# Kernel tuning notes

Measured on AMD Instinct MI355X. Metric: run time of the kernel, lower is better.

## Reference

```python
import jax, jax.numpy as jnp
import numpy as np

# --- model dims (from init args) ---
LAYERS = 6
LEAF = 2 ** (LAYERS - 1)        # 32
M_LEN = 128
CAM_NUM = 2
MAIN_CAM = 0
LATENT = 48
H_LAT = 2048                    # LatentNet hidden
H_BR = 512                      # ChooseBranchNet hidden
B = 16384

# Path bits: for leaf i, bit at classifier depth d (root->leaf order) is
# (i >> (LAYERS-2-d)) & 1. This is exactly what the search_table + double
# advanced-indexing gather in the torch code computes (heap tree routing).
_BITS = ((np.arange(LEAF)[:, None] >> np.arange(LAYERS - 2, -1, -1)[None, :]) & 1)  # [LEAF, LAYERS-1]
BITS = jnp.asarray(_BITS, dtype=jnp.int32)


def setup_inputs() -> dict:
    key = jax.random.key(0)
    ks = jax.random.split(key, 9)
    s = lambda fan: 1.0 / np.sqrt(fan)
    return {
        "batch_data": jax.random.normal(ks[0], (B, CAM_NUM, M_LEN), dtype=jnp.float32),
        # LatentNet: [B, 2*M_LEN] -> hidden -> LEAF*LATENT
        "Wl1": jax.random.normal(ks[1], (2 * M_LEN, H_LAT), dtype=jnp.float32) * s(2 * M_LEN),
        "bl1": jnp.zeros((H_LAT,), dtype=jnp.float32),
        "Wl2": jax.random.normal(ks[2], (H_LAT, LEAF * LATENT), dtype=jnp.float32) * s(H_LAT),
        "bl2": jnp.zeros((LEAF * LATENT,), dtype=jnp.float32),
        # ChooseBranchNet (shared across the LAYERS-1 classifier slots): M_LEN -> hidden -> 2
        "Wb1": jax.random.normal(ks[3], (M_LEN, H_BR), dtype=jnp.float32) * s(M_LEN),
        "bb1": jnp.zeros((H_BR,), dtype=jnp.float32),
        "Wb2": jax.random.normal(ks[4], (H_BR, 2), dtype=jnp.float32) * s(H_BR),
        "bb2": jnp.zeros((2,), dtype=jnp.float32),
    }


def reference(batch_data, Wl1, bl1, Wl2, bl2, Wb1, bb1, Wb2, bb2):
    bsz = batch_data.shape[0]
    # expand_measurements: main cam repeated (LAYERS-1) times -> [B, LAYERS-1, M_LEN]
    main = batch_data[:, MAIN_CAM]                                  # [B, M_LEN]
    x_br = jnp.broadcast_to(main[:, None, :], (bsz, LAYERS - 1, M_LEN))
    # ChooseBranchNet -> per-layer 2-way probabilities
    h = jax.nn.relu(jnp.einsum('blm,mh->blh', x_br, Wb1) + bb1)
    p = jax.nn.softmax(jnp.einsum('blh,ho->blo', h, Wb2) + bb2, axis=-1)  # [B, L-1, 2]
    # Tree gates: product of path-branch probabilities along root->leaf path.
    comp = jnp.where(BITS[None] == 1, p[:, None, :, 1], p[:, None, :, 0])  # [B, LEAF, L-1]
    gates = jnp.prod(comp, axis=-1)                                        # [B, LEAF]
    # top-1 routing (argsort(...)[:, -1] as in the torch code)
    router = jnp.argsort(gates, axis=-1)[:, -1]                            # [B]
    # LatentNet on concatenated two-camera measurements
    x2 = jnp.concatenate([batch_data[:, 0], batch_data[:, 1]], axis=-1)    # [B, 2*M_LEN]
    hl = jax.nn.relu(x2 @ Wl1 + bl1)
    nn_latent = (hl @ Wl2 + bl2).reshape(bsz, LEAF, LATENT)
    # scatter-select per-sample leaf latent (replaces the torch.where loop)
    select = jnp.take_along_axis(nn_latent, router[:, None, None], axis=1)[:, 0]  # [B, LATENT]
    return select
```

## Files before the change

kernel.cpp:

```cpp
#include <hip/hip_runtime.h>
#include <stdint.h>

typedef short bf16x8 __attribute__((ext_vector_type(8)));
typedef float f32x4 __attribute__((ext_vector_type(4)));

#define NROWS 16384
#define K1DIM 256
#define N1DIM 2048
#define N2DIM 96
#define MARGIN 0.03f

#define GLD16(g, l) __builtin_amdgcn_global_load_lds( \
    (const __attribute__((address_space(1))) uint32_t*)(g), \
    (__attribute__((address_space(3))) uint32_t*)(l), 16, 0, 0)

__device__ __forceinline__ ushort f2bf(float x) {
  union { float f; uint32_t u; } c; c.f = x;
  uint32_t u = c.u;
  return (ushort)((u + 0x7FFFu + ((u >> 16) & 1u)) >> 16);
}

__global__ __launch_bounds__(256) void k0_convert(
    const float* __restrict__ bd, const float* __restrict__ Wl1,
    const float* __restrict__ Wl2, const float* __restrict__ Wb1,
    ushort* __restrict__ x2bf, ushort* __restrict__ wl1t,
    ushort* __restrict__ w2t, ushort* __restrict__ wb1t) {
  int i = blockIdx.x * 256 + threadIdx.x;
  {
    float4 v = ((const float4*)bd)[i];
    ushort4 o;
    o.x = f2bf(v.x); o.y = f2bf(v.y); o.z = f2bf(v.z); o.w = f2bf(v.w);
    ((ushort4*)x2bf)[i] = o;
  }
  if (i < 2048 * 256) {
    int n = i >> 8, k = i & 255;
    wl1t[i] = f2bf(Wl1[k * 2048 + n]);
  }
  if (i < 96 * 2048) {
    int j = i >> 11, k = i & 2047;
    int col = (j < 48) ? j : (1440 + j);
    w2t[i] = f2bf(Wl2[k * 1536 + col]);
  }
  if (i < 512 * 128) {
    int j = i >> 7, m = i & 127;
    wb1t[i] = f2bf(Wb1[m * 512 + j]);
  }
}

__global__ __launch_bounds__(256) void k1a_score(
    const ushort* __restrict__ x2bf, const ushort* __restrict__ wb1t,
    const float* __restrict__ bb1, const float* __restrict__ Wb2,
    float* __restrict__ part) {
  __shared__ __align__(1024) ushort As[128 * 64];
  __shared__ __align__(1024) ushort Bs[128 * 64];
  const int t = threadIdx.x, ln = t & 63, wv = t >> 6;
  const int m0 = blockIdx.y << 7;
  const int n0 = blockIdx.x << 7;
  const int wm = (wv >> 1) << 6, wn = (wv & 1) << 6;
  const int rsub = ln >> 3, kc8 = ln & 7;
  const int q = ln >> 4, rr = ln & 15;

  f32x4 acc[4][4] = {};

  for (int k0 = 0; k0 < 128; k0 += 64) {
#pragma unroll
    for (int i = 0; i < 4; i++) {
      int inst = (wv << 2) + i;
      int row = (inst << 3) + rsub;
      GLD16(x2bf + (size_t)(m0 + row) * 256 + k0 + (kc8 << 3), As + (inst << 9));
      GLD16(wb1t + (size_t)(n0 + row) * 128 + k0 + (kc8 << 3), Bs + (inst << 9));
    }
    __syncthreads();
#pragma unroll
    for (int kk = 0; kk < 2; kk++) {
      int kb = ((kk << 2) + q) << 3;
      bf16x8 af[4], bfr[4];
#pragma unroll
      for (int mi = 0; mi < 4; mi++)
        af[mi] = *(const bf16x8*)(As + (((wm + (mi << 4) + rr)) << 6) + kb);
#pragma unroll
      for (int ni = 0; ni < 4; ni++)
        bfr[ni] = *(const bf16x8*)(Bs + (((wn + (ni << 4) + rr)) << 6) + kb);
#pragma unroll
      for (int mi = 0; mi < 4; mi++)
#pragma unroll
        for (int ni = 0; ni < 4; ni++)
          acc[mi][ni] = __builtin_amdgcn_mfma_f32_16x16x32_bf16(
              af[mi], bfr[ni], acc[mi][ni], 0, 0, 0);
    }
    __syncthreads();
  }

  float s4[4][4] = {};
#pragma unroll
  for (int ni = 0; ni < 4; ni++) {
    int col = n0 + wn + (ni << 4) + rr;
    float bias = bb1[col];
    float wdv = Wb2[col * 2 + 1] - Wb2[col * 2];
#pragma unroll
    for (int mi = 0; mi < 4; mi++) {
      f32x4 a = acc[mi][ni];
#pragma unroll
      for (int v = 0; v < 4; v++)
        s4[mi][v] += fmaxf(a[v] + bias, 0.f) * wdv;
    }
  }
#pragma unroll
  for (int off = 1; off <= 8; off <<= 1)
#pragma unroll
    for (int mi = 0; mi < 4; mi++)
#pragma unroll
      for (int v = 0; v < 4; v++)
        s4[mi][v] += __shfl_xor(s4[mi][v], off);

  if (rr == 0) {
    float* dst = part + (size_t)(blockIdx.x * 2 + (wv & 1)) * NROWS +
                 m0 + wm + (q << 2);
#pragma unroll
    for (int mi = 0; mi < 4; mi++) {
      float4 v4 = make_float4(s4[mi][0], s4[mi][1], s4[mi][2], s4[mi][3]);
      *(float4*)(dst + (mi << 4)) = v4;
    }
  }
}

__global__ __launch_bounds__(256) void k1b_classify(
    const float* __restrict__ part, const float* __restrict__ bb2,
    int* __restrict__ router, int* __restrict__ list, int* __restrict__ counter) {
  int t = blockIdx.x * 256 + threadIdx.x;
  float s = bb2[1] - bb2[0];
#pragma unroll
  for (int i = 0; i < 8; i++) s += part[i * NROWS + t];
  router[t] = (s >= 0.f) ? 1 : 0;
  if (fabsf(s) < MARGIN) {
    int idx = atomicAdd(counter, 1);
    list[idx] = t;
  }
}

__global__ __launch_bounds__(256) void k1c_recheck(
    const float* __restrict__ bd, const float* __restrict__ Wb1,
    const float* __restrict__ Wb2, const float* __restrict__ bb1,
    const float* __restrict__ bb2, const int* __restrict__ list,
    const int* __restrict__ counter, int* __restrict__ router) {
  const int ln = threadIdx.x & 63;
  const int wid = (blockIdx.x * 256 + threadIdx.x) >> 6;
  const int count = *counter;
  const float c = bb2[1] - bb2[0];

  for (int base = wid * 4; base < count; base += 512 * 4) {
    int rows[4];
#pragma unroll
    for (int r = 0; r < 4; r++) {
      int idx = base + r;
      rows[r] = list[(idx < count) ? idx : base];
    }
    float acc[4][8];
#pragma unroll
    for (int r = 0; r < 4; r++)
#pragma unroll
      for (int u = 0; u < 8; u++) acc[r][u] = 0.f;

    for (int m = 0; m < 128; m++) {
      float w[8];
#pragma unroll
      for (int u = 0; u < 8; u++) w[u] = Wb1[m * 512 + (u << 6) + ln];
#pragma unroll
      for (int r = 0; r < 4; r++) {
        float x = bd[(size_t)rows[r] * 256 + m];
#pragma unroll
        for (int u = 0; u < 8; u++) acc[r][u] = fmaf(x, w[u], acc[r][u]);
      }
    }
    float sc[4];
#pragma unroll
    for (int r = 0; r < 4; r++) {
      float s = 0.f;
#pragma unroll
      for (int u = 0; u < 8; u++) {
        int j = (u << 6) + ln;
        float wd = Wb2[j * 2 + 1] - Wb2[j * 2];
        s += fmaxf(acc[r][u] + bb1[j], 0.f) * wd;
      }
#pragma unroll
      for (int off = 1; off <= 32; off <<= 1) s += __shfl_xor(s, off);
      sc[r] = s + c;
    }
    if (ln == 0) {
#pragma unroll
      for (int r = 0; r < 4; r++)
        if (base + r < count) router[rows[r]] = (sc[r] >= 0.f) ? 1 : 0;
    }
  }
}

__global__ __launch_bounds__(256, 2) void k2_fused(
    const ushort* __restrict__ x2bf, const ushort* __restrict__ wl1t,
    const ushort* __restrict__ w2t, const float* __restrict__ bl1,
    const float* __restrict__ bl2, const int* __restrict__ router,
    float* __restrict__ out) {
  __shared__ __align__(1024) ushort Bsm[16384];
  __shared__ __align__(1024) ushort Asm[8192];
  __shared__ __align__(1024) ushort Wsm[12288];
  ushort* Hs = Bsm;
  const int t = threadIdx.x, ln = t & 63, wv = t >> 6;
  const int ks2 = blockIdx.x;
  const int m0 = blockIdx.y << 6;
  const int q = ln >> 4, rr = ln & 15;
  const int sr4 = ln >> 4;
  const int s16 = ln & 15;

  f32x4 accP[6] = {};

  for (int nc = 0; nc < 8; nc++) {
    const int n0 = (ks2 << 10) + (nc << 7);

#pragma unroll
    for (int j = 0; j < 6; j++) {
      int inst = wv * 6 + j;
      int r = (inst << 2) + sr4;
      int c = s16 ^ (r & 7);
      GLD16(w2t + (size_t)r * 2048 + n0 + (c << 3), Wsm + (inst << 9));
    }

    f32x4 acc1[4][2] = {};
#pragma unroll 1
    for (int ks = 0; ks < 2; ks++) {
      const int kg = ks << 7;
#pragma unroll
      for (int i = 0; i < 4; i++) {
        int inst = (wv << 2) + i;
        int r = (inst << 2) + sr4;
        int c = s16 ^ (r & 7);
        GLD16(x2bf + (size_t)(m0 + r) * K1DIM + kg + (c << 3),
              Asm + (inst << 9));
      }
#pragma unroll
      for (int i = 0; i < 8; i++) {
        int inst = (wv << 3) + i;
        int r = (inst << 2) + sr4;
        int c = s16 ^ (r & 7);
        GLD16(wl1t + (size_t)(n0 + r) * K1DIM + kg + (c << 3),
              Bsm + (inst << 9));
      }
      __syncthreads();
#pragma unroll
      for (int kk = 0; kk < 4; kk++) {
        int c = (kk << 2) + q;
        int sl = (c ^ (rr & 7)) << 3;
        bf16x8 af[4], bfr[2];
#pragma unroll
        for (int mi = 0; mi < 4; mi++)
          af[mi] = *(const bf16x8*)(Asm + (((mi << 4) + rr) << 7) + sl);
#pragma unroll
        for (int ni = 0; ni < 2; ni++)
          bfr[ni] = *(const bf16x8*)(Bsm + (((wv << 5) + (ni << 4) + rr) << 7) + sl);
#pragma unroll
        for (int mi = 0; mi < 4; mi++)
#pragma unroll
          for (int ni = 0; ni < 2; ni++)
            acc1[mi][ni] = __builtin_amdgcn_mfma_f32_16x16x32_bf16(
                af[mi], bfr[ni], acc1[mi][ni], 0, 0, 0);
      }
      __syncthreads();
    }

#pragma unroll
    for (int ni = 0; ni < 2; ni++) {
      int col = (wv << 5) + (ni << 4) + rr;
      float bias = bl1[n0 + col];
#pragma unroll
      for (int mi = 0; mi < 4; mi++) {
        f32x4 a = acc1[mi][ni];
#pragma unroll
        for (int v = 0; v < 4; v++) {
          int row = (mi << 4) + (q << 2) + v;
          Hs[(row << 7) + (((col >> 3) ^ (row & 15)) << 3) + (col & 7)] =
              f2bf(fmaxf(a[v] + bias, 0.f));
        }
      }
    }
    __syncthreads();

#pragma unroll
    for (int kk = 0; kk < 4; kk++) {
      int cH = (kk << 2) + q;
      bf16x8 ha = *(const bf16x8*)(Hs + (((wv << 4) + rr) << 7) +
                                   ((cH ^ rr) << 3));
#pragma unroll
      for (int ni = 0; ni < 6; ni++) {
        bf16x8 wb = *(const bf16x8*)(Wsm + (((ni << 4) + rr) << 7) +
                                     ((cH ^ (rr & 7)) << 3));
        accP[ni] = __builtin_amdgcn_mfma_f32_16x16x32_bf16(ha, wb, accP[ni], 0, 0, 0);
      }
    }
    __syncthreads();
  }

  {
    int rowb = m0 + (wv << 4) + (q << 2);
#pragma unroll
    for (int v = 0; v < 4; v++) {
      int row = rowb + v;
      int sel = router[row];
      float v0 = sel ? accP[3][v] : accP[0][v];
      float v1 = sel ? accP[4][v] : accP[1][v];
      float v2 = sel ? accP[5][v] : accP[2][v];
      if (ks2 == 0) {
        int bb = sel ? 1488 : 0;
        v0 += bl2[bb + rr];
        v1 += bl2[bb + 16 + rr];
        v2 += bl2[bb + 32 + rr];
      }
      float* ob = out + (size_t)row * 48 + rr;
      atomicAdd(ob, v0);
      atomicAdd(ob + 16, v1);
      atomicAdd(ob + 32, v2);
    }
  }
}

extern "C" void kernel_launch(void* const* d_in, const int* in_sizes, int n_in,
                              void* d_out, int out_size, void* d_ws, size_t ws_size,
                              hipStream_t stream) {
  const float* bd  = (const float*)d_in[0];
  const float* Wl1 = (const float*)d_in[1];
  const float* bl1 = (const float*)d_in[2];
  const float* Wl2 = (const float*)d_in[3];
  const float* bl2 = (const float*)d_in[4];
  const float* Wb1 = (const float*)d_in[5];
  const float* bb1 = (const float*)d_in[6];
  const float* Wb2 = (const float*)d_in[7];
  const float* bb2 = (const float*)d_in[8];

  char* ws = (char*)d_ws;
  ushort* x2bf  = (ushort*)(ws);
  ushort* wl1t  = (ushort*)(ws + 8388608);
  ushort* w2t   = (ushort*)(ws + 9437184);
  int*    router= (int*)(ws + 89522176);
  ushort* wb1t  = (ushort*)(ws + 89587712);
  float*  part  = (float*)(ws + 89718784);
  int*    list  = (int*)(ws + 90243072);
  int*    counter=(int*)(ws + 90308608);
  float*  outp  = (float*)d_out;

  k0_convert<<<dim3(4096), dim3(256), 0, stream>>>(bd, Wl1, Wl2, Wb1,
                                                   x2bf, wl1t, w2t, wb1t);
  hipMemsetAsync(counter, 0, 4, stream);
  hipMemsetAsync(outp, 0, (size_t)out_size * 4, stream);
  k1a_score<<<dim3(4, 128), dim3(256), 0, stream>>>(x2bf, wb1t, bb1, Wb2, part);
  k1b_classify<<<dim3(64), dim3(256), 0, stream>>>(part, bb2, router, list, counter);
  k1c_recheck<<<dim3(128), dim3(256), 0, stream>>>(bd, Wb1, Wb2, bb1, bb2,
                                                   list, counter, router);
  k2_fused<<<dim3(2, 256), dim3(256), 0, stream>>>(x2bf, wl1t, w2t, bl1, bl2,
                                                   router, outp);
}
```

Baseline: 170.8 us.

## Keep full A tile resident in LDS and stream Wl1 fragments directly from global

The fused kernel now loads the block's full 64x256 activation tile into LDS once instead of re-staging it per N chunk. Wl1 fragments are read straight from global memory into registers, with a wider 64-column-per-wave tile, so the Wl1 LDS staging and its barriers go away. The second GEMM is split into two 128-column halves, and the waves are repartitioned so each computes only one candidate leaf's outputs and writes atomics only for matching rows. The risk is higher global-load latency on the uncached Wl1 reads and more accumulator registers, which could lower occupancy.

```diff
diff --git a/kernel.cpp b/kernel.cpp
--- a/kernel.cpp
+++ b/kernel.cpp
@@ -199,123 +199,125 @@
     const ushort* __restrict__ w2t, const float* __restrict__ bl1,
     const float* __restrict__ bl2, const int* __restrict__ router,
     float* __restrict__ out) {
-  __shared__ __align__(1024) ushort Bsm[16384];
-  __shared__ __align__(1024) ushort Asm[8192];
-  __shared__ __align__(1024) ushort Wsm[12288];
-  ushort* Hs = Bsm;
+  __shared__ __align__(1024) ushort As[64 * 256];
+  __shared__ __align__(1024) ushort Hs[64 * 128];
+  __shared__ __align__(1024) ushort Wsm[96 * 128];
   const int t = threadIdx.x, ln = t & 63, wv = t >> 6;
   const int ks2 = blockIdx.x;
   const int m0 = blockIdx.y << 6;
   const int q = ln >> 4, rr = ln & 15;
-  const int sr4 = ln >> 4;
-  const int s16 = ln & 15;
-
-  f32x4 accP[6] = {};
-
-  for (int nc = 0; nc < 8; nc++) {
-    const int n0 = (ks2 << 10) + (nc << 7);
-
-#pragma unroll
-    for (int j = 0; j < 6; j++) {
-      int inst = wv * 6 + j;
-      int r = (inst << 2) + sr4;
-      int c = s16 ^ (r & 7);
-      GLD16(w2t + (size_t)r * 2048 + n0 + (c << 3), Wsm + (inst << 9));
-    }
-
-    f32x4 acc1[4][2] = {};
+  const int rg = wv & 1, cg = wv >> 1;
+
+  {
+    int s = ln & 31, rh = ln >> 5;
+#pragma unroll
+    for (int i = 0; i < 8; i++) {
+      int inst = (wv << 3) + i;
+      int r = (inst << 1) + rh;
+      GLD16(x2bf + (size_t)(m0 + r) * 256 + ((s ^ (r & 31)) << 3),
+            As + (inst << 9));
+    }
+  }
+  __syncthreads();
+
+  f32x4 accP[2][3] = {};
+
+  for (int nc = 0; nc < 4; nc++) {
+    const int n0 = (ks2 << 10) + (nc << 8);
+    const int nw = n0 + (wv << 6);
+
+    f32x4 acc1[4][4] = {};
+#pragma unroll 4
+    for (int kk = 0; kk < 8; kk++) {
+      bf16x8 bfr[4];
+#pragma unroll
+      for (int ni = 0; ni < 4; ni++)
+        bfr[ni] = *(const bf16x8*)(wl1t + (size_t)(nw + (ni << 4) + rr) * 256 +
+                                   (kk << 5) + (q << 3));
+      bf16x8 af[4];
+#pragma unroll
+      for (int mi = 0; mi < 4; mi++) {
+        int row = (mi << 4) + rr;
+        af[mi] = *(const bf16x8*)(As + (row << 8) +
+                                  ((((kk << 2) + q) ^ (row & 31)) << 3));
+      }
+#pragma unroll
+      for (int mi = 0; mi < 4; mi++)
+#pragma unroll
+        for (int ni = 0; ni < 4; ni++)
+          acc1[mi][ni] = __builtin_amdgcn_mfma_f32_16x16x32_bf16(
+              af[mi], bfr[ni], acc1[mi][ni], 0, 0, 0);
+    }
+
 #pragma unroll 1
-    for (int ks = 0; ks < 2; ks++) {
-      const int kg = ks << 7;
-#pragma unroll
-      for (int i = 0; i < 4; i++) {
-        int inst = (wv << 2) + i;
-        int r = (inst << 2) + sr4;
-        int c = s16 ^ (r & 7);
-        GLD16(x2bf + (size_t)(m0 + r) * K1DIM + kg + (c << 3),
-              Asm + (inst << 9));
-      }
-#pragma unroll
-      for (int i = 0; i < 8; i++) {
-        int inst = (wv << 3) + i;
-        int r = (inst << 2) + sr4;
-        int c = s16 ^ (r & 7);
-        GLD16(wl1t + (size_t)(n0 + r) * K1DIM + kg + (c << 3),
-              Bsm + (inst << 9));
+    for (int h = 0; h < 2; h++) {
+#pragma unroll
+      for (int j = 0; j < 6; j++) {
+        int inst = wv * 6 + j;
+        int r = (inst << 2) + q;
+        GLD16(w2t + (size_t)r * 2048 + n0 + (h << 7) + ((rr ^ (r & 15)) << 3),
+              Wsm + (inst << 9));
+      }
+      if ((wv >> 1) == h) {
+#pragma unroll
+        for (int ni = 0; ni < 4; ni++) {
+          int colh = ((wv & 1) << 6) + (ni << 4) + rr;
+          float bias = bl1[nw + (ni << 4) + rr];
+#pragma unroll
+          for (int mi = 0; mi < 4; mi++) {
+            f32x4 a = acc1[mi][ni];
+#pragma unroll
+            for (int v = 0; v < 4; v++) {
+              int row = (mi << 4) + (q << 2) + v;
+              Hs[(row << 7) + (((colh >> 3) ^ (row & 15)) << 3) + (colh & 7)] =
+                  f2bf(fmaxf(a[v] + bias, 0.f));
+            }
+          }
+        }
       }
       __syncthreads();
 #pragma unroll
       for (int kk = 0; kk < 4; kk++) {
         int c = (kk << 2) + q;
-        int sl = (c ^ (rr & 7)) << 3;
-        bf16x8 af[4], bfr[2];
-#pragma unroll
-        for (int mi = 0; mi < 4; mi++)
-          af[mi] = *(const bf16x8*)(Asm + (((mi << 4) + rr) << 7) + sl);
-#pragma unroll
-        for (int ni = 0; ni < 2; ni++)
-          bfr[ni] = *(const bf16x8*)(Bsm + (((wv << 5) + (ni << 4) + rr) << 7) + sl);
-#pragma unroll
-        for (int mi = 0; mi < 4; mi++)
-#pragma unroll
-          for (int ni = 0; ni < 2; ni++)
-            acc1[mi][ni] = __builtin_amdgcn_mfma_f32_16x16x32_bf16(
-                af[mi], bfr[ni], acc1[mi][ni], 0, 0, 0);
+        bf16x8 ha[2];
+#pragma unroll
+        for (int a = 0; a < 2; a++) {
+          int row = (rg << 5) + (a << 4) + rr;
+          ha[a] = *(const bf16x8*)(Hs + (row << 7) + ((c ^ rr) << 3));
+        }
+#pragma unroll
+        for (int ni = 0; ni < 3; ni++) {
+          int jr = cg * 48 + (ni << 4) + rr;
+          bf16x8 wb = *(const bf16x8*)(Wsm + (jr << 7) + ((c ^ rr) << 3));
+#pragma unroll
+          for (int a = 0; a < 2; a++)
+            accP[a][ni] = __builtin_amdgcn_mfma_f32_16x16x32_bf16(
+                ha[a], wb, accP[a][ni], 0, 0, 0);
+        }
       }
       __syncthreads();
     }
-
-#pragma unroll
-    for (int ni = 0; ni < 2; ni++) {
-      int col = (wv << 5) + (ni << 4) + rr;
-      float bias = bl1[n0 + col];
-#pragma unroll
-      for (int mi = 0; mi < 4; mi++) {
-        f32x4 a = acc1[mi][ni];
-#pragma unroll
-        for (int v = 0; v < 4; v++) {
-          int row = (mi << 4) + (q << 2) + v;
-          Hs[(row << 7) + (((col >> 3) ^ (row & 15)) << 3) + (col & 7)] =
-              f2bf(fmaxf(a[v] + bias, 0.f));
+  }
+
+#pragma unroll
+  for (int a = 0; a < 2; a++) {
+#pragma unroll
+    for (int v = 0; v < 4; v++) {
+      int row = m0 + (rg << 5) + (a << 4) + (q << 2) + v;
+      int sel = router[row];
+      if (sel == cg) {
+        float b0 = 0.f, b1 = 0.f, b2 = 0.f;
+        if (ks2 == 0) {
+          int bb = sel ? 1488 : 0;
+          b0 = bl2[bb + rr];
+          b1 = bl2[bb + 16 + rr];
+          b2 = bl2[bb + 32 + rr];
         }
-      }
-    }
-    __syncthreads();
-
-#pragma unroll
-    for (int kk = 0; kk < 4; kk++) {
-      int cH = (kk << 2) + q;
-      bf16x8 ha = *(const bf16x8*)(Hs + (((wv << 4) + rr) << 7) +
-                                   ((cH ^ rr) << 3));
-#pragma unroll
-      for (int ni = 0; ni < 6; ni++) {
-        bf16x8 wb = *(const bf16x8*)(Wsm + (((ni << 4) + rr) << 7) +
-                                     ((cH ^ (rr & 7)) << 3));
-        accP[ni] = __builtin_amdgcn_mfma_f32_16x16x32_bf16(ha, wb, accP[ni], 0, 0, 0);
-      }
-    }
-    __syncthreads();
-  }
-
-  {
-    int rowb = m0 + (wv << 4) + (q << 2);
-#pragma unroll
-    for (int v = 0; v < 4; v++) {
-      int row = rowb + v;
-      int sel = router[row];
-      float v0 = sel ? accP[3][v] : accP[0][v];
-      float v1 = sel ? accP[4][v] : accP[1][v];
-      float v2 = sel ? accP[5][v] : accP[2][v];
-      if (ks2 == 0) {
-        int bb = sel ? 1488 : 0;
-        v0 += bl2[bb + rr];
-        v1 += bl2[bb + 16 + rr];
-        v2 += bl2[bb + 32 + rr];
-      }
-      float* ob = out + (size_t)row * 48 + rr;
-      atomicAdd(ob, v0);
-      atomicAdd(ob + 16, v1);
-      atomicAdd(ob + 32, v2);
+        float* ob = out + (size_t)row * 48 + rr;
+        atomicAdd(ob, accP[a][0][v] + b0);
+        atomicAdd(ob + 16, accP[a][1][v] + b1);
+        atomicAdd(ob + 32, accP[a][2][v] + b2);
+      }
     }
   }
 }
```

Measured after the change: 183.2 us. 7.2% more time.
